# Optimization experiments

Hardware: AMD Instinct MI355X
Metric: run time of the kernel (lower is better)

## Reference

```python
import jax, jax.numpy as jnp
import numpy as np

B, T, IN = 256, 60, 520
GATE_IN = 8                      # 5 + 3, hard-coded in module
MOE_RAW = IN - GATE_IN           # 512
MOE_IN = MOE_RAW + GATE_IN * T   # 992
HID = MOE_RAW + (GATE_IN * T) // 2  # 752 (Python precedence: a + b*c//2)
OUT = 512
E = 8


def _uniform(key, shape, bound):
    return jax.random.uniform(key, shape, jnp.float32, -bound, bound)


def setup_inputs() -> dict:
    key = jax.random.key(0)
    ks = jax.random.split(key, 16)
    X = jax.random.normal(ks[0], (B, T, IN), jnp.float32)
    # GRU: 2 layers, hidden = E, gate order r,z,n (torch convention)
    gb = 1.0 / np.sqrt(E)
    Wih0 = _uniform(ks[1], (3 * E, GATE_IN), gb)
    Whh0 = _uniform(ks[2], (3 * E, E), gb)
    bih0 = _uniform(ks[3], (3 * E,), gb)
    bhh0 = _uniform(ks[4], (3 * E,), gb)
    Wih1 = _uniform(ks[5], (3 * E, E), gb)
    Whh1 = _uniform(ks[6], (3 * E, E), gb)
    bih1 = _uniform(ks[7], (3 * E,), gb)
    bhh1 = _uniform(ks[8], (3 * E,), gb)
    # Expert banks: glorot-style uniform as in init_params, zero biases
    def bank(k, i, o):
        wb = np.sqrt(6.0 / (i * o))
        return _uniform(k, (E, i, o), wb)
    w1 = bank(ks[9], MOE_IN, HID); b1 = jnp.zeros((E, HID), jnp.float32)
    w2 = bank(ks[10], HID, HID);   b2 = jnp.zeros((E, HID), jnp.float32)
    w3 = bank(ks[11], HID, OUT);   b3 = jnp.zeros((E, OUT), jnp.float32)
    return dict(X=X, Wih0=Wih0, Whh0=Whh0, bih0=bih0, bhh0=bhh0,
                Wih1=Wih1, Whh1=Whh1, bih1=bih1, bhh1=bhh1,
                w1=w1, b1=b1, w2=w2, b2=b2, w3=w3, b3=b3)


def _gru_layer(x, Wih, Whh, bih, bhh):
    # x: [B, T, in] -> outputs [B, T, H]
    H = Whh.shape[1]
    h0 = jnp.zeros((x.shape[0], H), x.dtype)

    def step(h, xt):
        gi = xt @ Wih.T + bih
        gh = h @ Whh.T + bhh
        ir, iz, i_n = jnp.split(gi, 3, axis=-1)
        hr, hz, h_n = jnp.split(gh, 3, axis=-1)
        r = jax.nn.sigmoid(ir + hr)
        z = jax.nn.sigmoid(iz + hz)
        n = jnp.tanh(i_n + r * h_n)
        h_new = (1.0 - z) * n + z * h
        return h_new, h_new

    _, ys = jax.lax.scan(step, h0, jnp.swapaxes(x, 0, 1))
    return jnp.swapaxes(ys, 0, 1)


def _blend_layer(x, coef, w, b):
    # per-sample weight synthesis + apply: same math as
    # sum(coef[...,None,None]*w[None],dim=1) then sum(x[...,None]*W,dim=1)+b
    Wb = jnp.einsum('be,eih->bih', coef, w)   # [B, in, out]
    bb = coef @ b                              # [B, out]
    return jnp.einsum('bi,bih->bh', x, Wb) + bb


def reference(X, Wih0, Whh0, bih0, bhh0, Wih1, Whh1, bih1, bhh1,
              w1, b1, w2, b2, w3, b3):
    Xg = X[:, :, MOE_RAW:]                                   # [B, T, 8]
    Xm = jnp.concatenate(
        [X[:, -1, :MOE_RAW], X[:, :, -GATE_IN:].reshape(X.shape[0], -1)], -1)
    # gating: 2-layer GRU, softmax on last step of layer 2
    h1 = _gru_layer(Xg, Wih0, Whh0, bih0, bhh0)
    h2 = _gru_layer(h1, Wih1, Whh1, bih1, bhh1)
    Omega = jax.nn.softmax(h2[:, -1, :], axis=-1)            # [B, E]
    # expert MLP with blended per-sample weights
    a = jax.nn.elu(_blend_layer(Xm, Omega, w1, b1))
    a = jax.nn.elu(_blend_layer(a, Omega, w2, b2))
    Y = _blend_layer(a, Omega, w3, b3)
    return Y
```

## Files before the change

kernel.cpp:

```cpp
#include <hip/hip_runtime.h>
#include <cstdint>
#include <cstddef>

typedef __attribute__((ext_vector_type(8))) short short8;
typedef __attribute__((ext_vector_type(8))) unsigned short ushort8;
typedef __attribute__((ext_vector_type(4))) float f32x4;

#define AS1Q const __attribute__((address_space(1)))
#define AS3Q __attribute__((address_space(3)))

constexpr int T_N = 60, IN_N = 520, MOE_RAW_N = 512, MOE_IN_N = 992;
constexpr int HID_N = 752, E_N = 8;
constexpr int K1_N = 7936, K2_N = 6016;
constexpr int SPLITK = 20;

static __device__ __forceinline__ unsigned short f2bf(float f) {
  unsigned int u = __float_as_uint(f);
  return (unsigned short)((u + 0x7fffu + ((u >> 16) & 1u)) >> 16);
}
static __device__ __forceinline__ float sigf(float x) {
  return __fdividef(1.f, 1.f + __expf(-x));
}
static __device__ __forceinline__ float tanh_fast(float x) {
  return 2.f * __fdividef(1.f, 1.f + __expf(-2.f * x)) - 1.f;
}

__global__ __launch_bounds__(64, 1)
void gru_omega_kernel(const float* __restrict__ X,
                      const float* __restrict__ Wih0, const float* __restrict__ Whh0,
                      const float* __restrict__ bih0, const float* __restrict__ bhh0,
                      const float* __restrict__ Wih1, const float* __restrict__ Whh1,
                      const float* __restrict__ bih1, const float* __restrict__ bhh1,
                      float* __restrict__ Omega)
{
  __shared__ float xl[T_N][8][8];

  const int lane = threadIdx.x;
  const int j = lane & 7;
  const int base = lane & 56;
  const int s = lane >> 3;
  const int b = blockIdx.x * 8 + s;

  const float* xsrc = X + (size_t)b * (T_N * IN_N) + MOE_RAW_N + j;
#pragma unroll
  for (int t = 0; t < T_N; ++t) {
    __builtin_amdgcn_global_load_lds((AS1Q unsigned int*)(xsrc + t * IN_N),
                                     (AS3Q unsigned int*)&xl[t][0][0], 4, 0, 0);
  }

  float wi0r[8], wi0z[8], wi0n[8], wh0r[8], wh0z[8], wh0n[8];
  float wi1r[8], wi1z[8], wi1n[8], wh1r[8], wh1z[8], wh1n[8];
#pragma unroll
  for (int i = 0; i < 8; ++i) {
    wi0r[i] = Wih0[j * 8 + i]; wi0z[i] = Wih0[(8 + j) * 8 + i]; wi0n[i] = Wih0[(16 + j) * 8 + i];
    wh0r[i] = Whh0[j * 8 + i]; wh0z[i] = Whh0[(8 + j) * 8 + i]; wh0n[i] = Whh0[(16 + j) * 8 + i];
    wi1r[i] = Wih1[j * 8 + i]; wi1z[i] = Wih1[(8 + j) * 8 + i]; wi1n[i] = Wih1[(16 + j) * 8 + i];
    wh1r[i] = Whh1[j * 8 + i]; wh1z[i] = Whh1[(8 + j) * 8 + i]; wh1n[i] = Whh1[(16 + j) * 8 + i];
  }
  const float br0 = bih0[j] + bhh0[j], bz0 = bih0[8 + j] + bhh0[8 + j];
  const float bin0 = bih0[16 + j],     bhn0 = bhh0[16 + j];
  const float br1 = bih1[j] + bhh1[j], bz1 = bih1[8 + j] + bhh1[8 + j];
  const float bin1 = bih1[16 + j],     bhn1 = bhh1[16 + j];

  __syncthreads();

  float h1 = 0.f, h2 = 0.f;
  float bh1[8], bh2[8];
#pragma unroll
  for (int i = 0; i < 8; ++i) { bh1[i] = 0.f; bh2[i] = 0.f; }

#pragma unroll 1
  for (int t = 0; t < T_N; ++t) {
    const f32x4 x0 = *(const f32x4*)&xl[t][s][0];
    const f32x4 x1 = *(const f32x4*)&xl[t][s][4];

    float gr = br0, gz = bz0, gn = bin0, hn = bhn0;
#pragma unroll
    for (int i = 0; i < 4; ++i) {
      gr += wi0r[i] * x0[i]; gz += wi0z[i] * x0[i]; gn += wi0n[i] * x0[i];
      gr += wi0r[4 + i] * x1[i]; gz += wi0z[4 + i] * x1[i]; gn += wi0n[4 + i] * x1[i];
    }
#pragma unroll
    for (int i = 0; i < 8; ++i) {
      gr += wh0r[i] * bh1[i]; gz += wh0z[i] * bh1[i]; hn += wh0n[i] * bh1[i];
    }
    float r = sigf(gr), z = sigf(gz);
    float n = tanh_fast(gn + r * hn);
    h1 = (1.f - z) * n + z * h1;

#pragma unroll
    for (int i = 0; i < 8; ++i) bh1[i] = __shfl(h1, base + i);

    gr = br1; gz = bz1; gn = bin1; hn = bhn1;
#pragma unroll
    for (int i = 0; i < 8; ++i) {
      gr += wi1r[i] * bh1[i]; gz += wi1z[i] * bh1[i]; gn += wi1n[i] * bh1[i];
    }
#pragma unroll
    for (int i = 0; i < 8; ++i) {
      gr += wh1r[i] * bh2[i]; gz += wh1z[i] * bh2[i]; hn += wh1n[i] * bh2[i];
    }
    r = sigf(gr); z = sigf(gz);
    n = tanh_fast(gn + r * hn);
    h2 = (1.f - z) * n + z * h2;

#pragma unroll
    for (int i = 0; i < 8; ++i) bh2[i] = __shfl(h2, base + i);
  }

  float m = h2;
#pragma unroll
  for (int d = 1; d < 8; d <<= 1) m = fmaxf(m, __shfl_xor(m, d));
  float e = __expf(h2 - m);
  float sden = e;
#pragma unroll
  for (int d = 1; d < 8; d <<= 1) sden += __shfl_xor(sden, d);
  Omega[b * 8 + j] = __fdividef(e, sden);
}

__global__ __launch_bounds__(256)
void mix1_kernel(const float* __restrict__ X, const float* __restrict__ Omega,
                 unsigned short* __restrict__ xt1)
{
  const int idx = blockIdx.x * 256 + threadIdx.x;
  const int b = idx / MOE_IN_N;
  const int i = idx - b * MOE_IN_N;
  const float* Xb = X + (size_t)b * (T_N * IN_N);
  float xm;
  if (i < MOE_RAW_N) {
    xm = Xb[(T_N - 1) * IN_N + i];
  } else {
    const int t = (i - MOE_RAW_N) >> 3, g = (i - MOE_RAW_N) & 7;
    xm = Xb[t * IN_N + MOE_RAW_N + g];
  }
  const int swz = (b & 7) << 3;
  unsigned short* row = xt1 + (size_t)b * K1_N;
#pragma unroll
  for (int e = 0; e < 8; ++e) {
    float w = Omega[b * 8 + e];
    row[(e * MOE_IN_N + i) ^ swz] = f2bf(w * xm);
  }
}

__global__ __launch_bounds__(256)
void gemm_splitk(const unsigned short* __restrict__ A,
                 const float* __restrict__ Bw,
                 float* __restrict__ P,
                 int K, int N, int NPAD)
{
  __shared__ unsigned short Al[2][256][64];
  __shared__ unsigned short Bl[2][64][64];

  const int tid = threadIdx.x;
  const int lane = tid & 63;
  const int wave = tid >> 6;
  const int nt = blockIdx.x, sp = blockIdx.y;
  const int n0 = nt * 64;
  const int KT = K >> 6;
  const int kt0 = (KT * sp) / SPLITK;
  const int kt1 = (KT * (sp + 1)) / SPLITK;

  const int r15 = lane & 15, hi4 = lane >> 4, r7 = lane & 7;

  const unsigned short* Abase = A + (size_t)(wave * 64 + (lane >> 3)) * K + (lane & 7) * 8;
  const int bn = lane;
  const int kq = wave;
  const bool nvalid = (n0 + bn) < N;
  const float* Bbase = Bw + (size_t)(kq * 16) * N + (n0 + bn);

  f32x4 acc[4][4];
  const f32x4 zero4 = {0.f, 0.f, 0.f, 0.f};
#pragma unroll
  for (int mi = 0; mi < 4; ++mi)
#pragma unroll
    for (int ni = 0; ni < 4; ++ni) acc[mi][ni] = zero4;

  auto stage = [&](int bufi, int kt) {
    const unsigned short* ga = Abase + kt * 64;
#pragma unroll
    for (int it = 0; it < 8; ++it) {
      __builtin_amdgcn_global_load_lds(
          (AS1Q unsigned int*)(ga + (size_t)it * 8 * K),
          (AS3Q unsigned int*)&Al[bufi][wave * 64 + it * 8][0],
          16, 0, 0);
    }
    const float* gb = Bbase + (size_t)kt * 64 * N;
    float v[16];
#pragma unroll
    for (int jj = 0; jj < 16; ++jj) v[jj] = nvalid ? gb[(size_t)jj * N] : 0.f;
    ushort8 p0, p1;
#pragma unroll
    for (int jj = 0; jj < 8; ++jj) { p0[jj] = f2bf(v[jj]); p1[jj] = f2bf(v[jj + 8]); }
    const int sl0 = ((kq * 2) ^ (bn & 7)) * 8;
    const int sl1 = ((kq * 2 + 1) ^ (bn & 7)) * 8;
    *(ushort8*)&Bl[bufi][bn][sl0] = p0;
    *(ushort8*)&Bl[bufi][bn][sl1] = p1;
  };

  auto compute = [&](int bufi) {
#pragma unroll
    for (int ki = 0; ki < 2; ++ki) {
      const int ch = ((ki * 4 + hi4) ^ r7) * 8;
      short8 af[4], bfv[4];
#pragma unroll
      for (int mi = 0; mi < 4; ++mi)
        af[mi] = *(const short8*)&Al[bufi][wave * 64 + mi * 16 + r15][ch];
#pragma unroll
      for (int ni = 0; ni < 4; ++ni)
        bfv[ni] = *(const short8*)&Bl[bufi][ni * 16 + r15][ch];
#pragma unroll
      for (int mi = 0; mi < 4; ++mi)
#pragma unroll
        for (int ni = 0; ni < 4; ++ni)
          acc[mi][ni] = __builtin_amdgcn_mfma_f32_16x16x32_bf16(af[mi], bfv[ni], acc[mi][ni], 0, 0, 0);
    }
  };

  stage(0, kt0);
  __syncthreads();
  int buf = 0;
  for (int kt = kt0; kt < kt1; ++kt) {
    if (kt + 1 < kt1) stage(buf ^ 1, kt + 1);
    compute(buf);
    __syncthreads();
    buf ^= 1;
  }

  float* Pp = P + (size_t)sp * 256 * NPAD + n0;
#pragma unroll
  for (int mi = 0; mi < 4; ++mi) {
    const int row = wave * 64 + mi * 16 + hi4 * 4;
#pragma unroll
    for (int ni = 0; ni < 4; ++ni) {
#pragma unroll
      for (int rr = 0; rr < 4; ++rr)
        Pp[(size_t)(row + rr) * NPAD + ni * 16 + r15] = acc[mi][ni][rr];
    }
  }
}

__global__ __launch_bounds__(256)
void reduce_mix_kernel(const float* __restrict__ P, const float* __restrict__ Omega,
                       const float* __restrict__ bias, unsigned short* __restrict__ xnext,
                       float* __restrict__ Yout, int N, int NPAD)
{
  const int n = blockIdx.x * 256 + threadIdx.x;
  const int b = blockIdx.y;
  if (n >= N) return;
  float acc = 0.f;
#pragma unroll 4
  for (int s = 0; s < SPLITK; ++s) acc += P[((size_t)s * 256 + b) * NPAD + n];
  float om[8];
#pragma unroll
  for (int e = 0; e < 8; ++e) om[e] = Omega[b * 8 + e];
  float bs = 0.f;
#pragma unroll
  for (int e = 0; e < 8; ++e) bs += om[e] * bias[(size_t)e * N + n];
  float y = acc + bs;
  if (Yout) { Yout[(size_t)b * N + n] = y; return; }
  float a = (y > 0.f) ? y : expm1f(y);
  const int swz = (b & 7) << 3;
  unsigned short* row = xnext + (size_t)b * K2_N;
#pragma unroll
  for (int e = 0; e < 8; ++e)
    row[(e * HID_N + n) ^ swz] = f2bf(om[e] * a);
}

extern "C" void kernel_launch(void* const* d_in, const int* in_sizes, int n_in,
                              void* d_out, int out_size, void* d_ws, size_t ws_size,
                              hipStream_t stream) {
  const float* X    = (const float*)d_in[0];
  const float* Wih0 = (const float*)d_in[1];
  const float* Whh0 = (const float*)d_in[2];
  const float* bih0 = (const float*)d_in[3];
  const float* bhh0 = (const float*)d_in[4];
  const float* Wih1 = (const float*)d_in[5];
  const float* Whh1 = (const float*)d_in[6];
  const float* bih1 = (const float*)d_in[7];
  const float* bhh1 = (const float*)d_in[8];
  const float* w1   = (const float*)d_in[9];
  const float* b1   = (const float*)d_in[10];
  const float* w2   = (const float*)d_in[11];
  const float* b2   = (const float*)d_in[12];
  const float* w3   = (const float*)d_in[13];
  const float* b3   = (const float*)d_in[14];

  char* ws = (char*)d_ws;
  float* Omega        = (float*)ws;
  unsigned short* xt1 = (unsigned short*)(ws + 8192);
  unsigned short* xt2 = (unsigned short*)(ws + 8192 + 4063232);
  unsigned short* xt3 = (unsigned short*)(ws + 8192 + 4063232 + 3080192);
  float* P            = (float*)(ws + 8192 + 4063232 + 3080192 + 3080192);

  gru_omega_kernel<<<32, 64, 0, stream>>>(X, Wih0, Whh0, bih0, bhh0,
                                          Wih1, Whh1, bih1, bhh1, Omega);
  mix1_kernel<<<992, 256, 0, stream>>>(X, Omega, xt1);

  gemm_splitk<<<dim3(12, SPLITK), 256, 0, stream>>>(xt1, w1, P, K1_N, HID_N, 768);
  reduce_mix_kernel<<<dim3(3, 256), 256, 0, stream>>>(P, Omega, b1, xt2, nullptr, HID_N, 768);

  gemm_splitk<<<dim3(12, SPLITK), 256, 0, stream>>>(xt2, w2, P, K2_N, HID_N, 768);
  reduce_mix_kernel<<<dim3(3, 256), 256, 0, stream>>>(P, Omega, b2, xt3, nullptr, HID_N, 768);

  gemm_splitk<<<dim3(8, SPLITK), 256, 0, stream>>>(xt3, w3, P, K2_N, 512, 512);
  reduce_mix_kernel<<<dim3(2, 256), 256, 0, stream>>>(P, Omega, b3, nullptr, (float*)d_out, 512, 512);
}
```

Baseline: 97.97 us.

## Use DPP row rotations instead of shuffles in GRU recurrence

The GRU gating kernel now broadcasts hidden and input values within each 8-lane group using DPP row_ror rotations instead of ds_bpermute shuffles. Weights are pre-permuted to match the rotation order, and a runtime check picks the rotation direction. Each wave now handles 4 samples with duplicated 8-lane halves, so the grid doubles to 64 blocks, and FMA chains are split into two accumulators to shorten dependency latency. The aim is to cut per-step latency on the serial 60-step recurrence, at the cost of half the lanes doing redundant work.

```diff
diff --git a/kernel.cpp b/kernel.cpp
--- a/kernel.cpp
+++ b/kernel.cpp
@@ -23,6 +23,17 @@
 }
 static __device__ __forceinline__ float tanh_fast(float x) {
   return 2.f * __fdividef(1.f, 1.f + __expf(-2.f * x)) - 1.f;
+}
+
+template<int R>
+static __device__ __forceinline__ float rotf(float v) {
+  return __int_as_float(__builtin_amdgcn_update_dpp(
+      0, __float_as_int(v), 0x120 | R, 0xF, 0xF, true));
+}
+static __device__ __forceinline__ void rot8(float (&d)[8], float v) {
+  d[0] = v;
+  d[1] = rotf<1>(v); d[2] = rotf<2>(v); d[3] = rotf<3>(v);
+  d[4] = rotf<4>(v); d[5] = rotf<5>(v); d[6] = rotf<6>(v); d[7] = rotf<7>(v);
 }
 
 __global__ __launch_bounds__(64, 1)
@@ -33,29 +44,32 @@
                       const float* __restrict__ bih1, const float* __restrict__ bhh1,
                       float* __restrict__ Omega)
 {
-  __shared__ float xl[T_N][8][8];
+  __shared__ float xl[T_N][64];
 
   const int lane = threadIdx.x;
   const int j = lane & 7;
-  const int base = lane & 56;
-  const int s = lane >> 3;
-  const int b = blockIdx.x * 8 + s;
+  const int s = lane >> 4;
+  const int b = blockIdx.x * 4 + s;
 
   const float* xsrc = X + (size_t)b * (T_N * IN_N) + MOE_RAW_N + j;
 #pragma unroll
   for (int t = 0; t < T_N; ++t) {
     __builtin_amdgcn_global_load_lds((AS1Q unsigned int*)(xsrc + t * IN_N),
-                                     (AS3Q unsigned int*)&xl[t][0][0], 4, 0, 0);
-  }
+                                     (AS3Q unsigned int*)&xl[t][0], 4, 0, 0);
+  }
+
+  const int got = __builtin_amdgcn_update_dpp(0, j, 0x121, 0xF, 0xF, true);
+  const bool plus = (got == ((j + 1) & 7));
 
   float wi0r[8], wi0z[8], wi0n[8], wh0r[8], wh0z[8], wh0n[8];
   float wi1r[8], wi1z[8], wi1n[8], wh1r[8], wh1z[8], wh1n[8];
 #pragma unroll
-  for (int i = 0; i < 8; ++i) {
-    wi0r[i] = Wih0[j * 8 + i]; wi0z[i] = Wih0[(8 + j) * 8 + i]; wi0n[i] = Wih0[(16 + j) * 8 + i];
-    wh0r[i] = Whh0[j * 8 + i]; wh0z[i] = Whh0[(8 + j) * 8 + i]; wh0n[i] = Whh0[(16 + j) * 8 + i];
-    wi1r[i] = Wih1[j * 8 + i]; wi1z[i] = Wih1[(8 + j) * 8 + i]; wi1n[i] = Wih1[(16 + j) * 8 + i];
-    wh1r[i] = Whh1[j * 8 + i]; wh1z[i] = Whh1[(8 + j) * 8 + i]; wh1n[i] = Whh1[(16 + j) * 8 + i];
+  for (int r = 0; r < 8; ++r) {
+    const int i = plus ? ((j + r) & 7) : ((j - r) & 7);
+    wi0r[r] = Wih0[j * 8 + i]; wi0z[r] = Wih0[(8 + j) * 8 + i]; wi0n[r] = Wih0[(16 + j) * 8 + i];
+    wh0r[r] = Whh0[j * 8 + i]; wh0z[r] = Whh0[(8 + j) * 8 + i]; wh0n[r] = Whh0[(16 + j) * 8 + i];
+    wi1r[r] = Wih1[j * 8 + i]; wi1z[r] = Wih1[(8 + j) * 8 + i]; wi1n[r] = Wih1[(16 + j) * 8 + i];
+    wh1r[r] = Whh1[j * 8 + i]; wh1z[r] = Whh1[(8 + j) * 8 + i]; wh1n[r] = Whh1[(16 + j) * 8 + i];
   }
   const float br0 = bih0[j] + bhh0[j], bz0 = bih0[8 + j] + bhh0[8 + j];
   const float bin0 = bih0[16 + j],     bhn0 = bhh0[16 + j];
@@ -65,57 +79,61 @@
   __syncthreads();
 
   float h1 = 0.f, h2 = 0.f;
-  float bh1[8], bh2[8];
-#pragma unroll
-  for (int i = 0; i < 8; ++i) { bh1[i] = 0.f; bh2[i] = 0.f; }
+  float xcur = xl[0][lane];
 
 #pragma unroll 1
   for (int t = 0; t < T_N; ++t) {
-    const f32x4 x0 = *(const f32x4*)&xl[t][s][0];
-    const f32x4 x1 = *(const f32x4*)&xl[t][s][4];
-
-    float gr = br0, gz = bz0, gn = bin0, hn = bhn0;
-#pragma unroll
-    for (int i = 0; i < 4; ++i) {
-      gr += wi0r[i] * x0[i]; gz += wi0z[i] * x0[i]; gn += wi0n[i] * x0[i];
-      gr += wi0r[4 + i] * x1[i]; gz += wi0z[4 + i] * x1[i]; gn += wi0n[4 + i] * x1[i];
-    }
-#pragma unroll
-    for (int i = 0; i < 8; ++i) {
-      gr += wh0r[i] * bh1[i]; gz += wh0z[i] * bh1[i]; hn += wh0n[i] * bh1[i];
-    }
-    float r = sigf(gr), z = sigf(gz);
-    float n = tanh_fast(gn + r * hn);
-    h1 = (1.f - z) * n + z * h1;
-
-#pragma unroll
-    for (int i = 0; i < 8; ++i) bh1[i] = __shfl(h1, base + i);
-
-    gr = br1; gz = bz1; gn = bin1; hn = bhn1;
-#pragma unroll
-    for (int i = 0; i < 8; ++i) {
-      gr += wi1r[i] * bh1[i]; gz += wi1z[i] * bh1[i]; gn += wi1n[i] * bh1[i];
-    }
-#pragma unroll
-    for (int i = 0; i < 8; ++i) {
-      gr += wh1r[i] * bh2[i]; gz += wh1z[i] * bh2[i]; hn += wh1n[i] * bh2[i];
-    }
-    r = sigf(gr); z = sigf(gz);
-    n = tanh_fast(gn + r * hn);
-    h2 = (1.f - z) * n + z * h2;
-
-#pragma unroll
-    for (int i = 0; i < 8; ++i) bh2[i] = __shfl(h2, base + i);
-  }
-
-  float m = h2;
-#pragma unroll
-  for (int d = 1; d < 8; d <<= 1) m = fmaxf(m, __shfl_xor(m, d));
-  float e = __expf(h2 - m);
-  float sden = e;
-#pragma unroll
-  for (int d = 1; d < 8; d <<= 1) sden += __shfl_xor(sden, d);
-  Omega[b * 8 + j] = __fdividef(e, sden);
+    const float xnext = xl[(t + 1 < T_N) ? t + 1 : t][lane];
+
+    float rx[8]; rot8(rx, xcur);
+    float rh[8]; rot8(rh, h1);
+    float grA = br0, gzA = bz0, gnA = bin0, hnA = bhn0;
+    float grB = 0.f, gzB = 0.f, gnB = 0.f, hnB = 0.f;
+#pragma unroll
+    for (int r = 0; r < 4; ++r) {
+      grA += wi0r[r] * rx[r];     gzA += wi0z[r] * rx[r];     gnA += wi0n[r] * rx[r];
+      grA += wh0r[r] * rh[r];     gzA += wh0z[r] * rh[r];     hnA += wh0n[r] * rh[r];
+      grB += wi0r[4+r] * rx[4+r]; gzB += wi0z[4+r] * rx[4+r]; gnB += wi0n[4+r] * rx[4+r];
+      grB += wh0r[4+r] * rh[4+r]; gzB += wh0z[4+r] * rh[4+r]; hnB += wh0n[4+r] * rh[4+r];
+    }
+    {
+      const float gr = grA + grB, gz = gzA + gzB, gn = gnA + gnB, hn = hnA + hnB;
+      const float r0 = sigf(gr), z0 = sigf(gz);
+      const float n0 = tanh_fast(gn + r0 * hn);
+      h1 = (1.f - z0) * n0 + z0 * h1;
+    }
+
+    float ri[8]; rot8(ri, h1);
+    float rh2[8]; rot8(rh2, h2);
+    float grA1 = br1, gzA1 = bz1, gnA1 = bin1, hnA1 = bhn1;
+    float grB1 = 0.f, gzB1 = 0.f, gnB1 = 0.f, hnB1 = 0.f;
+#pragma unroll
+    for (int r = 0; r < 4; ++r) {
+      grA1 += wi1r[r] * ri[r];     gzA1 += wi1z[r] * ri[r];     gnA1 += wi1n[r] * ri[r];
+      grA1 += wh1r[r] * rh2[r];    gzA1 += wh1z[r] * rh2[r];    hnA1 += wh1n[r] * rh2[r];
+      grB1 += wi1r[4+r] * ri[4+r]; gzB1 += wi1z[4+r] * ri[4+r]; gnB1 += wi1n[4+r] * ri[4+r];
+      grB1 += wh1r[4+r] * rh2[4+r];gzB1 += wh1z[4+r] * rh2[4+r];hnB1 += wh1n[4+r] * rh2[4+r];
+    }
+    {
+      const float gr = grA1 + grB1, gz = gzA1 + gzB1, gn = gnA1 + gnB1, hn = hnA1 + hnB1;
+      const float r1 = sigf(gr), z1 = sigf(gz);
+      const float n1 = tanh_fast(gn + r1 * hn);
+      h2 = (1.f - z1) * n1 + z1 * h2;
+    }
+
+    xcur = xnext;
+  }
+
+  float rv[8]; rot8(rv, h2);
+  float m = rv[0];
+#pragma unroll
+  for (int r = 1; r < 8; ++r) m = fmaxf(m, rv[r]);
+  const float ej = __expf(h2 - m);
+  float re[8]; rot8(re, ej);
+  float sden = 0.f;
+#pragma unroll
+  for (int r = 0; r < 8; ++r) sden += re[r];
+  if (!(lane & 8)) Omega[b * 8 + j] = __fdividef(ej, sden);
 }
 
 __global__ __launch_bounds__(256)
@@ -292,7 +310,7 @@
   unsigned short* xt3 = (unsigned short*)(ws + 8192 + 4063232 + 3080192);
   float* P            = (float*)(ws + 8192 + 4063232 + 3080192 + 3080192);
 
-  gru_omega_kernel<<<32, 64, 0, stream>>>(X, Wih0, Whh0, bih0, bhh0,
+  gru_omega_kernel<<<64, 64, 0, stream>>>(X, Wih0, Whh0, bih0, bhh0,
                                           Wih1, Whh1, bih1, bhh1, Omega);
   mix1_kernel<<<992, 256, 0, stream>>>(X, Omega, xt1);
 
```

After: 95.12 us. -2.9%, faster.
